# Kernel optimization log

Hardware: AMD Instinct MI355X
Metric: run time of the kernel (lower is better)

The kernel has to match this reference:

```python
import jax, jax.numpy as jnp
import numpy as np

N = 100000      # total nodes (100 graphs x 1000 nodes each)
G = 100         # graphs per batch
F_IN = 12       # node_features (temporal window)
F_OUT = 32      # DCRNN hidden size (hardcoded in module)
K = 5           # diffusion (Chebyshev) steps (hardcoded)
C = 4           # num_classes
E = 16 * N      # edges: ring (N) + random (15N)


def setup_inputs() -> dict:
    key = jax.random.key(0)
    ks = jax.random.split(key, 12)
    x = jax.random.normal(ks[0], (N, F_IN), dtype=jnp.float32)
    ring = jnp.arange(N, dtype=jnp.int32)
    src = jnp.concatenate([ring, jax.random.randint(ks[1], (15 * N,), 0, N, dtype=jnp.int32)])
    dst = jnp.concatenate([(ring + 1) % N, jax.random.randint(ks[2], (15 * N,), 0, N, dtype=jnp.int32)])
    edge_index = jnp.stack([src, dst])  # [2, E]
    edge_weight = jax.random.uniform(ks[3], (E,), dtype=jnp.float32, minval=0.1, maxval=1.0)
    batch = (jnp.arange(N, dtype=jnp.int32) * G) // N  # sorted graph ids, 1000 nodes per graph
    s = 0.1
    return dict(
        x=x, edge_index=edge_index, edge_weight=edge_weight, batch=batch,
        W_z=jax.random.normal(ks[4], (2, K, F_IN + F_OUT, F_OUT), jnp.float32) * s,
        b_z=jax.random.normal(ks[5], (F_OUT,), jnp.float32) * s,
        W_r=jax.random.normal(ks[6], (2, K, F_IN + F_OUT, F_OUT), jnp.float32) * s,
        b_r=jax.random.normal(ks[7], (F_OUT,), jnp.float32) * s,
        W_h=jax.random.normal(ks[8], (2, K, F_IN + F_OUT, F_OUT), jnp.float32) * s,
        b_h=jax.random.normal(ks[9], (F_OUT,), jnp.float32) * s,
        W_lin=jax.random.normal(ks[10], (F_OUT, C), jnp.float32) * s,
        b_lin=jax.random.normal(ks[11], (C,), jnp.float32) * s,
    )


def reference(x, edge_index, edge_weight, batch, W_z, b_z, W_r, b_r, W_h, b_h, W_lin, b_lin):
    row, col = edge_index[0], edge_index[1]
    # weighted in/out degrees (to_dense_adj sums duplicate edges, same as segment_sum)
    deg_out_inv = 1.0 / jax.ops.segment_sum(edge_weight, row, num_segments=N)
    deg_in_inv = 1.0 / jax.ops.segment_sum(edge_weight, col, num_segments=N)
    norm_out = deg_out_inv[row][:, None]  # per-edge 1/deg_out(src)
    norm_in = deg_in_inv[row][:, None]    # per-edge 1/deg_in(src), as in DConv

    def prop_fwd(h):  # out[dst] += h[src]/deg_out[src]
        return jax.ops.segment_sum(norm_out * h[row], col, num_segments=N)

    def prop_rev(h):  # reverse (transposed) diffusion: out[src] += h[dst]/deg_in[src]
        return jax.ops.segment_sum(norm_in * h[col], row, num_segments=N)

    def dconv(Xc, W, b):
        # Chebyshev diffusion conv, W: [2, K, F_in+F_out, F_out]
        H = Xc @ (W[0, 0] + W[1, 0])
        T1o, T1i = prop_fwd(Xc), prop_rev(Xc)
        H = H + T1o @ W[0, 1] + T1i @ W[1, 1]
        T0o = T0i = Xc
        for k in range(2, K):
            T2o = 2.0 * prop_fwd(T1o) - T0o
            T2i = 2.0 * prop_rev(T1i) - T0i
            H = H + T2o @ W[0, k] + T2i @ W[1, k]
            T0o, T1o = T1o, T2o
            T0i, T1i = T1i, T2i
        return H + b

    # GRU gating with zero-initialized hidden state (H=None in module)
    Hst = jnp.zeros((N, F_OUT), x.dtype)
    XH = jnp.concatenate([x, Hst], axis=1)
    Z = jax.nn.sigmoid(dconv(XH, W_z, b_z))
    R = jax.nn.sigmoid(dconv(XH, W_r, b_r))
    XRH = jnp.concatenate([x, R * Hst], axis=1)
    H_tilde = jnp.tanh(dconv(XRH, W_h, b_h))
    H = Z * Hst + (1.0 - Z) * H_tilde

    h = jax.nn.relu(H) @ W_lin + b_lin            # [N, C]
    sums = jax.ops.segment_sum(h, batch, num_segments=G)
    counts = jax.ops.segment_sum(jnp.ones((N,), h.dtype), batch, num_segments=G)
    return sums / counts[:, None]                 # global_mean_pool -> [G, C]
```

## Files before the change

kernel.cpp:

```cpp
#include <hip/hip_runtime.h>
#include <math.h>

#define NN    100000
#define GG    100
#define FIN   12
#define FOUT  32
#define KD    5
#define CC    4
#define EE    1600000
#define ROWS  108
#define NBF   782
#define NBINS 1564
#define NBC   512
#define CHUNK 3125
#define TOTR  (2 * CHUNK)
#define NSEG  (NBINS * NBC)
#define SUBMAX 3072

__device__ __forceinline__ unsigned bfr(float f) {
    unsigned u = __float_as_uint(f);
    return (u + 0x7FFFu + ((u >> 16) & 1u)) >> 16;
}
__device__ __forceinline__ unsigned pack2(float a, float b) {
    return bfr(a) | (bfr(b) << 16);
}
#define BLO(u) __uint_as_float((u) << 16)
#define BHI(u) __uint_as_float((u) & 0xFFFF0000u)

__device__ __forceinline__ int chunk_of_block(int b) {
    return ((b & 7) << 6) | (b >> 3);
}


__global__ __launch_bounds__(512) void k_hist(const int* __restrict__ ei,
                                              int* __restrict__ hist_g) {
    __shared__ int hist[NBINS];
    for (int i = threadIdx.x; i < NBINS; i += 512) hist[i] = 0;
    __syncthreads();
    int chunk = chunk_of_block(blockIdx.x);
    int lo = chunk * CHUNK, hi = lo + CHUNK;
    for (int e = lo + threadIdx.x; e < hi; e += 512) {
        int s = ei[e], d = ei[EE + e];
        atomicAdd(&hist[d >> 7], 1);
        atomicAdd(&hist[NBF + (s >> 7)], 1);
    }
    __syncthreads();
    for (int i = threadIdx.x; i < NBINS; i += 512)
        hist_g[i * NBC + chunk] = hist[i];
}

__global__ __launch_bounds__(1024) void k_scan1(
        int* __restrict__ g, int* __restrict__ bsum,
        const float* __restrict__ Wz_in, const float* __restrict__ Wh_in,
        float* __restrict__ Wz, float* __restrict__ Wh,
        const float* __restrict__ b_lin, float* __restrict__ out,
        const float* __restrict__ x, uint2* __restrict__ xb) {
    __shared__ int sh[1024];
    int t = threadIdx.x;
    int i = blockIdx.x * 1024 + t;
    int v = g[i];
    sh[t] = v;
    __syncthreads();
    for (int d = 1; d < 1024; d <<= 1) {
        int x2 = sh[t];
        if (t >= d) x2 += sh[t - d];
        __syncthreads();
        sh[t] = x2;
        __syncthreads();
    }
    g[i] = sh[t] - v;
    if (t == 1023) bsum[blockIdx.x] = sh[1023];

    if (i < 2 * ROWS * FOUT) {
        int sel = i / (ROWS * FOUT);
        int rem = i - sel * ROWS * FOUT;
        int r = rem / FOUT;
        int f = rem - r * FOUT;
        int b = r / 12;
        int ii = r - b * 12;
        const float* Ws = sel ? Wh_in : Wz_in;
        float vv;
        if (b == 0)
            vv = Ws[(0 * KD + 0) * 44 * 32 + ii * 32 + f] + Ws[(1 * KD + 0) * 44 * 32 + ii * 32 + f];
        else if (b <= 4)
            vv = Ws[(0 * KD + b) * 44 * 32 + ii * 32 + f];
        else
            vv = Ws[(1 * KD + (b - 4)) * 44 * 32 + ii * 32 + f];
        (sel ? Wh : Wz)[r * FOUT + f] = vv;
    }
    int u = i - 2 * ROWS * FOUT;
    if (u >= 0 && u < GG * CC) out[u] = b_lin[u & 3];
    if (i < 3 * NN) {
        int n = i / 3, c = i - n * 3;
        float4 vf = *(const float4*)(x + (size_t)n * FIN + c * 4);
        xb[(size_t)n * 3 + c] = make_uint2(pack2(vf.x, vf.y), pack2(vf.z, vf.w));
    }
}

__global__ __launch_bounds__(1024) void k_scan3(int* __restrict__ g,
                                                const int* __restrict__ bsum,
                                                int* __restrict__ off,
                                                int* __restrict__ off_node) {
    __shared__ int sh[1024];
    int t = threadIdx.x;
    sh[t] = (t < blockIdx.x) ? bsum[t] : 0;
    __syncthreads();
    for (int d = 512; d > 0; d >>= 1) {
        if (t < d) sh[t] += sh[t + d];
        __syncthreads();
    }
    int base = sh[0];
    int i = blockIdx.x * 1024 + t;
    int v = g[i] + base;
    g[i] = v;
    if ((i & (NBC - 1)) == 0) off[i / NBC] = v;
    if (i == 0) { off[NBINS] = 2 * EE; off_node[2 * NN] = 2 * EE; }
}

__global__ __launch_bounds__(512) void k_place(const int* __restrict__ ei,
                                               const float* __restrict__ ew,
                                               const int* __restrict__ base_g,
                                               int2* __restrict__ recA) {
    __shared__ int2 ldsrec[TOTR];
    __shared__ int  lofs[NBINS];
    __shared__ int  cur[NBINS];
    __shared__ int  sbase[NBINS];
    __shared__ unsigned short binof[TOTR];
    int* psum = (int*)binof;
    int t = threadIdx.x;
    int chunk = chunk_of_block(blockIdx.x);

    for (int bin = t; bin < NBINS; bin += 512) {
        int b0 = base_g[bin * NBC + chunk];
        int b1;
        if (chunk < NBC - 1)      b1 = base_g[bin * NBC + chunk + 1];
        else if (bin < NBINS - 1) b1 = base_g[(bin + 1) * NBC];
        else                      b1 = 2 * EE;
        sbase[bin] = b0;
        lofs[bin] = b1 - b0;
        cur[bin] = 0;
    }
    __syncthreads();

    int i0 = t * 4;
    int v0 = 0, v1 = 0, v2 = 0, v3 = 0;
    if (i0 + 0 < NBINS) v0 = lofs[i0];
    if (i0 + 1 < NBINS) v1 = lofs[i0 + 1];
    if (i0 + 2 < NBINS) v2 = lofs[i0 + 2];
    if (i0 + 3 < NBINS) v3 = lofs[i0 + 3];
    int s = v0 + v1 + v2 + v3;
    psum[t] = s;
    __syncthreads();
    for (int d = 1; d < 512; d <<= 1) {
        int x = psum[t];
        if (t >= d) x += psum[t - d];
        __syncthreads();
        psum[t] = x;
        __syncthreads();
    }
    int run = psum[t] - s;
    __syncthreads();
    if (i0 + 0 < NBINS) { lofs[i0]     = run; run += v0; }
    if (i0 + 1 < NBINS) { lofs[i0 + 1] = run; run += v1; }
    if (i0 + 2 < NBINS) { lofs[i0 + 2] = run; run += v2; }
    if (i0 + 3 < NBINS) { lofs[i0 + 3] = run; run += v3; }
    __syncthreads();

    int lo = chunk * CHUNK;
    for (int e = lo + t; e < lo + CHUNK; e += 512) {
        int s2 = ei[e], d2 = ei[EE + e];
        float w = ew[e];
        int bf = d2 >> 7;
        int pf = lofs[bf] + atomicAdd(&cur[bf], 1);
        ldsrec[pf] = make_int2(s2 | ((d2 & 127) << 17), __float_as_int(w));
        binof[pf] = (unsigned short)bf;
        int br = NBF + (s2 >> 7);
        int pr = lofs[br] + atomicAdd(&cur[br], 1);
        ldsrec[pr] = make_int2(d2 | ((s2 & 127) << 17), __float_as_int(w));
        binof[pr] = (unsigned short)br;
    }
    __syncthreads();

    for (int i = t; i < TOTR; i += 512) {
        int b = binof[i];
        recA[sbase[b] + (i - lofs[b])] = ldsrec[i];
    }
}

__global__ __launch_bounds__(256) void k_subcsr(
        const int* __restrict__ off, const int2* __restrict__ recA,
        const float* __restrict__ x,
        int* __restrict__ off_node, int* __restrict__ rec2,
        float* __restrict__ dinv_in, float* __restrict__ dinv_out,
        uint2* __restrict__ gA) {
    __shared__ int2  seg[SUBMAX];
    __shared__ int   hist[128];
    __shared__ int   lofs[128];
    __shared__ int   cur[128];
    __shared__ float wsum[128];
    __shared__ float dl[128];
    int b = blockIdx.x;
    int t = threadIdx.x;
    if (t < 128) { hist[t] = 0; wsum[t] = 0.f; }
    __syncthreads();
    int e0 = off[b], e1 = off[b + 1];
    int cnt = e1 - e0;
    bool stg = (cnt <= SUBMAX);
    if (stg) {
        for (int i = t; i < cnt; i += 256) {
            int2 r = recA[e0 + i];
            seg[i] = r;
            int loc = r.x >> 17;
            atomicAdd(&hist[loc], 1);
            atomicAdd(&wsum[loc], __int_as_float(r.y));
        }
    } else {
        for (int i = t; i < cnt; i += 256) {
            int2 r = recA[e0 + i];
            int loc = r.x >> 17;
            atomicAdd(&hist[loc], 1);
            atomicAdd(&wsum[loc], __int_as_float(r.y));
        }
    }
    __syncthreads();
    if (t < 128) lofs[t] = hist[t];
    __syncthreads();
    for (int d = 1; d < 128; d <<= 1) {
        int v = 0;
        if (t < 128 && t >= d) v = lofs[t - d];
        __syncthreads();
        if (t < 128) lofs[t] += v;
        __syncthreads();
    }
    bool rev = b >= NBF;
    int base = (rev ? b - NBF : b) * 128;
    if (t < 128) {
        int ex = lofs[t] - hist[t];
        lofs[t] = ex;
        cur[t] = 0;
        int node = base + t;
        if (node < NN) {
            off_node[(rev ? NN : 0) + node] = e0 + ex;
            float inv = 1.f / wsum[t];
            dl[t] = inv;
            if (rev) dinv_out[node] = inv;
            else     dinv_in[node]  = inv;
        }
    }
    __syncthreads();
    if (stg) {
        for (int i = t; i < cnt; i += 256) {
            int rx = seg[i].x;
            int loc = rx >> 17;
            int pos = e0 + lofs[loc] + atomicAdd(&cur[loc], 1);
            rec2[pos] = rx & 0x1FFFF;
        }
    } else {
        for (int i = t; i < cnt; i += 256) {
            int rx = recA[e0 + i].x;
            int loc = rx >> 17;
            int pos = e0 + lofs[loc] + atomicAdd(&cur[loc], 1);
            rec2[pos] = rx & 0x1FFFF;
        }
    }
    if (rev) {
        __syncthreads();
        for (int i = t; i < 128 * 3; i += 256) {
            int loc = i / 3, cc = i - loc * 3;
            int node = base + loc;
            if (node < NN) {
                float4 v = *(const float4*)(x + (size_t)node * FIN + cc * 4);
                float sc = dl[loc];
                gA[(size_t)node * 3 + cc] =
                    make_uint2(pack2(v.x * sc, v.y * sc), pack2(v.z * sc, v.w * sc));
            }
        }
    }
}

#define LREC 2048
__global__ __launch_bounds__(256) void k_gather(
        const int* __restrict__ off_node, const int* __restrict__ rec2,
        const uint2* __restrict__ gIn, const uint2* __restrict__ hIn,
        const uint2* __restrict__ prevF, const uint2* __restrict__ prevR,
        const float* __restrict__ dinv_in, const float* __restrict__ dinv_out,
        uint2* __restrict__ outF, uint2* __restrict__ outR,
        uint2* __restrict__ gOut, float c) {
    __shared__ int lrec[LREC];
    int xcd = blockIdx.x & 7;
    int grp = blockIdx.x >> 3;
    bool rev = xcd >= 4;
    int dbase = rev ? NN : 0;
    int ub = (grp * 4 + (xcd & 3)) * 256;
    int lin = ub + threadIdx.x;

    int u1 = ub + 255; if (u1 > 3 * NN - 1) u1 = 3 * NN - 1;
    int node0 = ub / 3, node1 = u1 / 3;
    int w0 = off_node[dbase + node0];
    int w1 = off_node[dbase + node1 + 1];
    int wn = w1 - w0;
    bool useLds = (wn <= LREC);
    if (useLds) {
        for (int i = threadIdx.x; i < wn; i += 256) lrec[i] = rec2[w0 + i];
    }
    __syncthreads();

    if (lin < 3 * NN) {
        int node = lin / 3;
        int ch = lin - node * 3;
        int i0 = dbase + node;
        int e0 = off_node[i0], e1 = off_node[i0 + 1];
        const uint2* in = rev ? hIn : gIn;

        float ax = 0.f, ay = 0.f, az = 0.f, aw = 0.f;
        float bx = 0.f, by = 0.f, bz = 0.f, bw = 0.f;
        if (useLds) {
            int a0 = e0 - w0, a1 = e1 - w0;
            int e = a0;
            for (; e + 7 < a1; e += 8) {
                int n0 = lrec[e],     n1 = lrec[e + 1], n2 = lrec[e + 2], n3 = lrec[e + 3];
                int n4 = lrec[e + 4], n5 = lrec[e + 5], n6 = lrec[e + 6], n7 = lrec[e + 7];
                uint2 v0 = in[(size_t)n0 * 3 + ch];
                uint2 v1 = in[(size_t)n1 * 3 + ch];
                uint2 v2 = in[(size_t)n2 * 3 + ch];
                uint2 v3 = in[(size_t)n3 * 3 + ch];
                uint2 v4 = in[(size_t)n4 * 3 + ch];
                uint2 v5 = in[(size_t)n5 * 3 + ch];
                uint2 v6 = in[(size_t)n6 * 3 + ch];
                uint2 v7 = in[(size_t)n7 * 3 + ch];
                ax += BLO(v0.x); ay += BHI(v0.x); az += BLO(v0.y); aw += BHI(v0.y);
                bx += BLO(v1.x); by += BHI(v1.x); bz += BLO(v1.y); bw += BHI(v1.y);
                ax += BLO(v2.x); ay += BHI(v2.x); az += BLO(v2.y); aw += BHI(v2.y);
                bx += BLO(v3.x); by += BHI(v3.x); bz += BLO(v3.y); bw += BHI(v3.y);
                ax += BLO(v4.x); ay += BHI(v4.x); az += BLO(v4.y); aw += BHI(v4.y);
                bx += BLO(v5.x); by += BHI(v5.x); bz += BLO(v5.y); bw += BHI(v5.y);
                ax += BLO(v6.x); ay += BHI(v6.x); az += BLO(v6.y); aw += BHI(v6.y);
                bx += BLO(v7.x); by += BHI(v7.x); bz += BLO(v7.y); bw += BHI(v7.y);
            }
            for (; e < a1; ++e) {
                int n0 = lrec[e];
                uint2 v0 = in[(size_t)n0 * 3 + ch];
                ax += BLO(v0.x); ay += BHI(v0.x); az += BLO(v0.y); aw += BHI(v0.y);
            }
        } else {
            for (int e = e0; e < e1; ++e) {
                int n0 = rec2[e];
                uint2 v0 = in[(size_t)n0 * 3 + ch];
                ax += BLO(v0.x); ay += BHI(v0.x); az += BLO(v0.y); aw += BHI(v0.y);
            }
        }
        ax += bx; ay += by; az += bz; aw += bw;

        float sc = rev ? c * dinv_in[node] : c;
        ax *= sc; ay *= sc; az *= sc; aw *= sc;

        size_t o = (size_t)node * 3 + ch;
        if (prevF) {
            uint2 p = (rev ? prevR : prevF)[o];
            ax -= BLO(p.x); ay -= BHI(p.x); az -= BLO(p.y); aw -= BHI(p.y);
        }
        (rev ? outR : outF)[o] = make_uint2(pack2(ax, ay), pack2(az, aw));
        if (!rev && gOut) {
            float g = dinv_out[node];
            gOut[o] = make_uint2(pack2(g * ax, g * ay), pack2(g * az, g * aw));
        }
    }
}


#define FREC 2560
__global__ __launch_bounds__(256) void k_fused(
        const float* __restrict__ x, const uint2* __restrict__ TS2,
        const int* __restrict__ off_node, const int* __restrict__ rec2,
        const uint2* __restrict__ gB, const float* __restrict__ dinv_in,
        const float* __restrict__ Wz, const float* __restrict__ Wh,
        const float* __restrict__ bz, const float* __restrict__ bh,
        const float* __restrict__ Wlin, float* __restrict__ out) {
    __shared__ float rows[128][13];
    __shared__ float red[256 * CC];
    __shared__ int   frec[FREC];
    int g = blockIdx.x >> 3;
    int seg = blockIdx.x & 7;
    int base = g * 1000 + seg * 125;
    int tid = threadIdx.x;
    int lane = tid & 63;
    int wave = tid >> 6;
    int f0 = __builtin_amdgcn_readfirstlane(wave * 8);

    const uint2* T2o = TS2 + (size_t)1 * NN * 3;
    const uint2* T2i = TS2 + (size_t)5 * NN * 3;
    const uint2* T3i = TS2 + (size_t)6 * NN * 3;

    float az0[8], ah0[8], az1[8], ah1[8];
#pragma unroll
    for (int fi = 0; fi < 8; ++fi) {
        float vz = bz[f0 + fi], vh = bh[f0 + fi];
        az0[fi] = vz; ah0[fi] = vh; az1[fi] = vz; ah1[fi] = vh;
    }
    bool act1 = (lane + 64) < 125;

    for (int b = 0; b < 9; ++b) {
        __syncthreads();
        if (b == 0) {
            const float* src = x + (size_t)base * FIN;
            for (int q = tid; q < 375; q += 256) {
                float4 v = *(const float4*)(src + q * 4);
                int e = q * 4;
                int n0 = e / 12,       i0 = e - n0 * 12;       rows[n0][i0] = v.x;
                int n1 = (e + 1) / 12, i1 = (e + 1) - n1 * 12; rows[n1][i1] = v.y;
                int n2 = (e + 2) / 12, i2 = (e + 2) - n2 * 12; rows[n2][i2] = v.z;
                int n3 = (e + 3) / 12, i3 = (e + 3) - n3 * 12; rows[n3][i3] = v.w;
            }
        } else if (b == 4 || b == 8) {
            bool revd = (b == 8);
            int dbase = revd ? NN : 0;
            const uint2* gin  = revd ? T3i : gB;
            const uint2* prev = revd ? T2i : T2o;
            int w0 = off_node[dbase + base];
            int w1 = off_node[dbase + base + 125];
            int wn = w1 - w0;
            bool useLds = (wn <= FREC);
            if (useLds) {
                for (int i = tid; i < wn; i += 256) frec[i] = rec2[w0 + i];
            }
            __syncthreads();
            for (int q = tid; q < 375; q += 256) {
                int n = q / 3, cc = q - n * 3;
                int node = base + n;
                int e0 = off_node[dbase + node], e1 = off_node[dbase + node + 1];
                float ax = 0.f, ay = 0.f, az = 0.f, aw = 0.f;
                if (useLds) {
#pragma unroll 4
                    for (int e = e0 - w0; e < e1 - w0; ++e) {
                        uint2 v = gin[(size_t)frec[e] * 3 + cc];
                        ax += BLO(v.x); ay += BHI(v.x); az += BLO(v.y); aw += BHI(v.y);
                    }
                } else {
                    for (int e = e0; e < e1; ++e) {
                        uint2 v = gin[(size_t)rec2[e] * 3 + cc];
                        ax += BLO(v.x); ay += BHI(v.x); az += BLO(v.y); aw += BHI(v.y);
                    }
                }
                float sc = revd ? 2.f * dinv_in[node] : 2.f;
                uint2 p = prev[(size_t)node * 3 + cc];
                rows[n][cc * 4 + 0] = ax * sc - BLO(p.x);
                rows[n][cc * 4 + 1] = ay * sc - BHI(p.x);
                rows[n][cc * 4 + 2] = az * sc - BLO(p.y);
                rows[n][cc * 4 + 3] = aw * sc - BHI(p.y);
            }
        } else {
            const uint2* Tb = TS2 + (size_t)(b - 1) * NN * 3;
            for (int q = tid; q < 375; q += 256) {
                int n = q / 3, cc = q - n * 3;
                uint2 v = Tb[(size_t)(base + n) * 3 + cc];
                rows[n][cc * 4 + 0] = BLO(v.x);
                rows[n][cc * 4 + 1] = BHI(v.x);
                rows[n][cc * 4 + 2] = BLO(v.y);
                rows[n][cc * 4 + 3] = BHI(v.y);
            }
        }
        __syncthreads();
        const float* wzr = Wz + b * 12 * FOUT + f0;
        const float* whr = Wh + b * 12 * FOUT + f0;
#pragma unroll
        for (int i = 0; i < FIN; ++i) {
            float v0 = rows[lane][i];
            float v1 = rows[lane + 64][i];
#pragma unroll
            for (int fi = 0; fi < 8; ++fi) {
                float wz = wzr[i * FOUT + fi];
                float wh = whr[i * FOUT + fi];
                az0[fi] = fmaf(v0, wz, az0[fi]);
                az1[fi] = fmaf(v1, wz, az1[fi]);
                ah0[fi] = fmaf(v0, wh, ah0[fi]);
                ah1[fi] = fmaf(v1, wh, ah1[fi]);
            }
        }
    }

    float o[CC] = {0.f, 0.f, 0.f, 0.f};
#pragma unroll
    for (int fi = 0; fi < 8; ++fi) {
        float z = 1.f / (1.f + __expf(-az0[fi]));
        float e2 = __expf(2.f * ah0[fi]);
        float th = 1.f - 2.f / (e2 + 1.f);
        float hv = fmaxf((1.f - z) * th, 0.f);
#pragma unroll
        for (int c = 0; c < CC; ++c) o[c] = fmaf(hv, Wlin[(f0 + fi) * 4 + c], o[c]);
    }
    if (act1) {
#pragma unroll
        for (int fi = 0; fi < 8; ++fi) {
            float z = 1.f / (1.f + __expf(-az1[fi]));
            float e2 = __expf(2.f * ah1[fi]);
            float th = 1.f - 2.f / (e2 + 1.f);
            float hv = fmaxf((1.f - z) * th, 0.f);
#pragma unroll
            for (int c = 0; c < CC; ++c) o[c] = fmaf(hv, Wlin[(f0 + fi) * 4 + c], o[c]);
        }
    }

#pragma unroll
    for (int c = 0; c < CC; ++c) red[tid * CC + c] = o[c];
    __syncthreads();
    for (int st = 128; st > 0; st >>= 1) {
        if (tid < st) {
#pragma unroll
            for (int c = 0; c < CC; ++c) red[tid * CC + c] += red[(tid + st) * CC + c];
        }
        __syncthreads();
    }
    if (tid == 0) {
#pragma unroll
        for (int c = 0; c < CC; ++c) atomicAdd(out + g * CC + c, red[c] * 0.001f);
    }
}


extern "C" void kernel_launch(void* const* d_in, const int* in_sizes, int n_in,
                              void* d_out, int out_size, void* d_ws, size_t ws_size,
                              hipStream_t stream) {
    const float* x     = (const float*)d_in[0];
    const int*   ei    = (const int*)d_in[1];
    const float* ew    = (const float*)d_in[2];
    const float* W_z   = (const float*)d_in[4];
    const float* b_z   = (const float*)d_in[5];
    const float* W_h   = (const float*)d_in[8];
    const float* b_h   = (const float*)d_in[9];
    const float* W_lin = (const float*)d_in[10];
    const float* b_lin = (const float*)d_in[11];
    float* out = (float*)d_out;

    int*   rec2     = (int*)d_ws;
    unsigned* TSb   = (unsigned*)(rec2 + 2 * (size_t)EE);
    int2*  recA     = (int2*)TSb;
    int*   hist_g   = rec2;
    int*   bsumS    = rec2 + NSEG;
    unsigned* gAu   = TSb + (size_t)8 * NN * 6 + 1600000;
    unsigned* gBu   = gAu + (size_t)NN * 6;
    unsigned* xbu   = gBu + (size_t)NN * 6;
    float* dinv_in  = (float*)(xbu + (size_t)NN * 6);
    float* dinv_out = dinv_in + NN;
    float* Wz       = dinv_out + NN;
    float* Wh       = Wz + ROWS * FOUT;
    int*   off      = (int*)(Wh + ROWS * FOUT);
    int*   off_node = off + NBINS + 1;

    uint2* TS2 = (uint2*)TSb;
    uint2* T1o = TS2 + (size_t)0 * NN * 3;
    uint2* T2o = TS2 + (size_t)1 * NN * 3;
    uint2* T3o = TS2 + (size_t)2 * NN * 3;
    uint2* T1i = TS2 + (size_t)4 * NN * 3;
    uint2* T2i = TS2 + (size_t)5 * NN * 3;
    uint2* T3i = TS2 + (size_t)6 * NN * 3;
    uint2* gA = (uint2*)gAu;
    uint2* gB = (uint2*)gBu;
    uint2* xb = (uint2*)xbu;

    dim3 B(256);
    int nbG = 2344;
    int nbScan = NSEG / 1024;

    k_hist<<<NBC, 512, 0, stream>>>(ei, hist_g);
    k_scan1<<<nbScan, 1024, 0, stream>>>(hist_g, bsumS, W_z, W_h, Wz, Wh, b_lin, out, x, xb);
    k_scan3<<<nbScan, 1024, 0, stream>>>(hist_g, bsumS, off, off_node);
    k_place<<<NBC, 512, 0, stream>>>(ei, ew, hist_g, recA);
    k_subcsr<<<NBINS, B, 0, stream>>>(off, recA, x, off_node, rec2, dinv_in, dinv_out, gA);

    k_gather<<<nbG, B, 0, stream>>>(off_node, rec2, gA, xb,  nullptr, nullptr, dinv_in, dinv_out, T1o, T1i, gB, 1.f);
    k_gather<<<nbG, B, 0, stream>>>(off_node, rec2, gB, T1i, xb,      xb,      dinv_in, dinv_out, T2o, T2i, gA, 2.f);
    k_gather<<<nbG, B, 0, stream>>>(off_node, rec2, gA, T2i, T1o,     T1i,     dinv_in, dinv_out, T3o, T3i, gB, 2.f);

    k_fused<<<8 * GG, B, 0, stream>>>(x, TS2, off_node, rec2, gB, dinv_in,
                                      Wz, Wh, b_z, b_h, W_lin, out);
}
```

Before: 283.6 us.

## Split fused GRU kernel into smaller node segments and unroll edge gather

The final fused kernel now processes 50 nodes per block instead of 125, launching 2000 blocks instead of 800, so each thread handles one node row and the register-doubled accumulators are dropped. The LDS-backed edge gather loop is unrolled by eight with two independent accumulator sets to raise memory-level parallelism. This targets low occupancy and long serial gather chains in the last kernel. The cost is more blocks reloading the weight rows, more partial-result reductions per graph, and a higher share of idle threads per block.

```diff
diff --git a/kernel.cpp b/kernel.cpp
--- a/kernel.cpp
+++ b/kernel.cpp
@@ -368,7 +368,9 @@
 }
 
 
-#define FREC 2560
+#define SEGN  50
+#define NSEGB 20
+#define FREC  1280
 __global__ __launch_bounds__(256) void k_fused(
         const float* __restrict__ x, const uint2* __restrict__ TS2,
         const int* __restrict__ off_node, const int* __restrict__ rec2,
@@ -376,36 +378,36 @@
         const float* __restrict__ Wz, const float* __restrict__ Wh,
         const float* __restrict__ bz, const float* __restrict__ bh,
         const float* __restrict__ Wlin, float* __restrict__ out) {
-    __shared__ float rows[128][13];
+    __shared__ float rows[64][13];
     __shared__ float red[256 * CC];
     __shared__ int   frec[FREC];
-    int g = blockIdx.x >> 3;
-    int seg = blockIdx.x & 7;
-    int base = g * 1000 + seg * 125;
+    int g = blockIdx.x / NSEGB;
+    int seg = blockIdx.x - g * NSEGB;
+    int base = g * 1000 + seg * SEGN;
     int tid = threadIdx.x;
     int lane = tid & 63;
     int wave = tid >> 6;
     int f0 = __builtin_amdgcn_readfirstlane(wave * 8);
+    bool act = lane < SEGN;
 
     const uint2* T2o = TS2 + (size_t)1 * NN * 3;
     const uint2* T2i = TS2 + (size_t)5 * NN * 3;
     const uint2* T3i = TS2 + (size_t)6 * NN * 3;
 
-    float az0[8], ah0[8], az1[8], ah1[8];
+    float az0[8], ah0[8];
 #pragma unroll
     for (int fi = 0; fi < 8; ++fi) {
-        float vz = bz[f0 + fi], vh = bh[f0 + fi];
-        az0[fi] = vz; ah0[fi] = vh; az1[fi] = vz; ah1[fi] = vh;
-    }
-    bool act1 = (lane + 64) < 125;
+        az0[fi] = bz[f0 + fi];
+        ah0[fi] = bh[f0 + fi];
+    }
 
     for (int b = 0; b < 9; ++b) {
         __syncthreads();
         if (b == 0) {
             const float* src = x + (size_t)base * FIN;
-            for (int q = tid; q < 375; q += 256) {
-                float4 v = *(const float4*)(src + q * 4);
-                int e = q * 4;
+            if (tid < 150) {
+                float4 v = *(const float4*)(src + tid * 4);
+                int e = tid * 4;
                 int n0 = e / 12,       i0 = e - n0 * 12;       rows[n0][i0] = v.x;
                 int n1 = (e + 1) / 12, i1 = (e + 1) - n1 * 12; rows[n1][i1] = v.y;
                 int n2 = (e + 2) / 12, i2 = (e + 2) - n2 * 12; rows[n2][i2] = v.z;
@@ -417,21 +419,43 @@
             const uint2* gin  = revd ? T3i : gB;
             const uint2* prev = revd ? T2i : T2o;
             int w0 = off_node[dbase + base];
-            int w1 = off_node[dbase + base + 125];
+            int w1 = off_node[dbase + base + SEGN];
             int wn = w1 - w0;
             bool useLds = (wn <= FREC);
             if (useLds) {
                 for (int i = tid; i < wn; i += 256) frec[i] = rec2[w0 + i];
             }
             __syncthreads();
-            for (int q = tid; q < 375; q += 256) {
-                int n = q / 3, cc = q - n * 3;
+            if (tid < 150) {
+                int n = tid / 3, cc = tid - n * 3;
                 int node = base + n;
                 int e0 = off_node[dbase + node], e1 = off_node[dbase + node + 1];
                 float ax = 0.f, ay = 0.f, az = 0.f, aw = 0.f;
+                float bx2 = 0.f, by2 = 0.f, bz2 = 0.f, bw2 = 0.f;
                 if (useLds) {
-#pragma unroll 4
-                    for (int e = e0 - w0; e < e1 - w0; ++e) {
+                    int a0 = e0 - w0, a1 = e1 - w0;
+                    int e = a0;
+                    for (; e + 7 < a1; e += 8) {
+                        int n0 = frec[e],     n1 = frec[e + 1], n2 = frec[e + 2], n3 = frec[e + 3];
+                        int n4 = frec[e + 4], n5 = frec[e + 5], n6 = frec[e + 6], n7 = frec[e + 7];
+                        uint2 v0 = gin[(size_t)n0 * 3 + cc];
+                        uint2 v1 = gin[(size_t)n1 * 3 + cc];
+                        uint2 v2 = gin[(size_t)n2 * 3 + cc];
+                        uint2 v3 = gin[(size_t)n3 * 3 + cc];
+                        uint2 v4 = gin[(size_t)n4 * 3 + cc];
+                        uint2 v5 = gin[(size_t)n5 * 3 + cc];
+                        uint2 v6 = gin[(size_t)n6 * 3 + cc];
+                        uint2 v7 = gin[(size_t)n7 * 3 + cc];
+                        ax += BLO(v0.x); ay += BHI(v0.x); az += BLO(v0.y); aw += BHI(v0.y);
+                        bx2 += BLO(v1.x); by2 += BHI(v1.x); bz2 += BLO(v1.y); bw2 += BHI(v1.y);
+                        ax += BLO(v2.x); ay += BHI(v2.x); az += BLO(v2.y); aw += BHI(v2.y);
+                        bx2 += BLO(v3.x); by2 += BHI(v3.x); bz2 += BLO(v3.y); bw2 += BHI(v3.y);
+                        ax += BLO(v4.x); ay += BHI(v4.x); az += BLO(v4.y); aw += BHI(v4.y);
+                        bx2 += BLO(v5.x); by2 += BHI(v5.x); bz2 += BLO(v5.y); bw2 += BHI(v5.y);
+                        ax += BLO(v6.x); ay += BHI(v6.x); az += BLO(v6.y); aw += BHI(v6.y);
+                        bx2 += BLO(v7.x); by2 += BHI(v7.x); bz2 += BLO(v7.y); bw2 += BHI(v7.y);
+                    }
+                    for (; e < a1; ++e) {
                         uint2 v = gin[(size_t)frec[e] * 3 + cc];
                         ax += BLO(v.x); ay += BHI(v.x); az += BLO(v.y); aw += BHI(v.y);
                     }
@@ -441,6 +465,7 @@
                         ax += BLO(v.x); ay += BHI(v.x); az += BLO(v.y); aw += BHI(v.y);
                     }
                 }
+                ax += bx2; ay += by2; az += bz2; aw += bw2;
                 float sc = revd ? 2.f * dinv_in[node] : 2.f;
                 uint2 p = prev[(size_t)node * 3 + cc];
                 rows[n][cc * 4 + 0] = ax * sc - BLO(p.x);
@@ -450,8 +475,8 @@
             }
         } else {
             const uint2* Tb = TS2 + (size_t)(b - 1) * NN * 3;
-            for (int q = tid; q < 375; q += 256) {
-                int n = q / 3, cc = q - n * 3;
+            if (tid < 150) {
+                int n = tid / 3, cc = tid - n * 3;
                 uint2 v = Tb[(size_t)(base + n) * 3 + cc];
                 rows[n][cc * 4 + 0] = BLO(v.x);
                 rows[n][cc * 4 + 1] = BHI(v.x);
@@ -465,34 +490,22 @@
 #pragma unroll
         for (int i = 0; i < FIN; ++i) {
             float v0 = rows[lane][i];
-            float v1 = rows[lane + 64][i];
 #pragma unroll
             for (int fi = 0; fi < 8; ++fi) {
                 float wz = wzr[i * FOUT + fi];
                 float wh = whr[i * FOUT + fi];
                 az0[fi] = fmaf(v0, wz, az0[fi]);
-                az1[fi] = fmaf(v1, wz, az1[fi]);
                 ah0[fi] = fmaf(v0, wh, ah0[fi]);
-                ah1[fi] = fmaf(v1, wh, ah1[fi]);
             }
         }
     }
 
     float o[CC] = {0.f, 0.f, 0.f, 0.f};
-#pragma unroll
-    for (int fi = 0; fi < 8; ++fi) {
-        float z = 1.f / (1.f + __expf(-az0[fi]));
-        float e2 = __expf(2.f * ah0[fi]);
-        float th = 1.f - 2.f / (e2 + 1.f);
-        float hv = fmaxf((1.f - z) * th, 0.f);
-#pragma unroll
-        for (int c = 0; c < CC; ++c) o[c] = fmaf(hv, Wlin[(f0 + fi) * 4 + c], o[c]);
-    }
-    if (act1) {
+    if (act) {
 #pragma unroll
         for (int fi = 0; fi < 8; ++fi) {
-            float z = 1.f / (1.f + __expf(-az1[fi]));
-            float e2 = __expf(2.f * ah1[fi]);
+            float z = 1.f / (1.f + __expf(-az0[fi]));
+            float e2 = __expf(2.f * ah0[fi]);
             float th = 1.f - 2.f / (e2 + 1.f);
             float hv = fmaxf((1.f - z) * th, 0.f);
 #pragma unroll
@@ -571,6 +584,6 @@
     k_gather<<<nbG, B, 0, stream>>>(off_node, rec2, gB, T1i, xb,      xb,      dinv_in, dinv_out, T2o, T2i, gA, 2.f);
     k_gather<<<nbG, B, 0, stream>>>(off_node, rec2, gA, T2i, T1o,     T1i,     dinv_in, dinv_out, T3o, T3i, gB, 2.f);
 
-    k_fused<<<8 * GG, B, 0, stream>>>(x, TS2, off_node, rec2, gB, dinv_in,
-                                      Wz, Wh, b_z, b_h, W_lin, out);
-}
+    k_fused<<<NSEGB * GG, B, 0, stream>>>(x, TS2, off_node, rec2, gB, dinv_in,
+                                          Wz, Wh, b_z, b_h, W_lin, out);
+}
```

Result: slower. 299.9 us (+5.7%).
